# Kernel optimization log

Hardware: AMD Instinct MI355X
Metric: run time of the kernel (lower is better)

The kernel has to match this reference:

```python
import jax, jax.numpy as jnp
import numpy as np

N, C, H, W = 128, 1024, 16, 16
D_IN, L, D_OUT, NQ = 2048, 512, 1024, 16


def setup_inputs() -> dict:
    key = jax.random.key(0)
    k1, k2, k3, k4, k5 = jax.random.split(key, 5)
    return {
        "cat_tensor": jax.random.normal(k1, (N, C, H, W), dtype=jnp.float32),
        "context": jax.random.normal(k2, (N, D_IN, L), dtype=jnp.float32),
        "query": jax.random.normal(k3, (1, NQ, D_IN), dtype=jnp.float32),
        "W_in": jax.random.normal(k4, (D_IN, D_IN), dtype=jnp.float32) * (1.0 / np.sqrt(D_IN)),
        "W_out": jax.random.normal(k5, (D_OUT, 2 * D_IN), dtype=jnp.float32) * (1.0 / np.sqrt(2 * D_IN)),
    }


def reference(cat_tensor, context, query, W_in, W_out):
    n, c, h, w = cat_tensor.shape
    # AttnBlock: context comes in as [N, D_in, L] -> transpose to [N, L, D_in]
    ctx = jnp.swapaxes(context, 1, 2)  # [N, L, D]
    # learned query broadcast over batch, then 'general' projection (Linear, no bias)
    q = jnp.einsum('nqd,ed->nqe', jnp.broadcast_to(query, (n,) + query.shape[1:]), W_in)  # [N, Q, D]
    scores = jnp.einsum('nqd,nld->nql', q, ctx)            # [N, Q, L]
    weights = jax.nn.softmax(scores, axis=-1)              # [N, Q, L]
    mix = jnp.einsum('nql,nld->nqd', weights, ctx)         # [N, Q, D]
    combined = jnp.concatenate([mix, q], axis=-1)          # [N, Q, 2D]
    out = jnp.tanh(jnp.einsum('nqe,oe->nqo', combined, W_out))  # [N, Q, D_out]
    # reshape queries to a small spatial map: [N, D_out, Hq, Hq]
    hq = int(np.sqrt(out.shape[1]))
    amap = jnp.swapaxes(out, 1, 2).reshape(n, out.shape[2], hq, hq)
    # F.interpolate(..., (H, W)) default mode='nearest': idx = floor(i * in / out)
    ih = (jnp.arange(h) * hq) // h
    iw = (jnp.arange(w) * hq) // w
    amap = amap[:, :, ih, :][:, :, :, iw]                  # [N, D_out, H, W]
    return jnp.concatenate([cat_tensor, amap], axis=1)     # [N, C + D_out, H, W]
```

## Files before the change

### kernel.cpp

```cpp
#include <hip/hip_runtime.h>
#include <hip/hip_bf16.h>

#define NB   128
#define CIN  1024
#define HW   256
#define DIN  2048
#define LL   512
#define DOUT 1024
#define NQ   16

#define SC   8

typedef __attribute__((ext_vector_type(8))) short bf16x8;
typedef __attribute__((ext_vector_type(4))) float f32x4;

__global__ __launch_bounds__(256) void k_q(const float* __restrict__ query,
                                           const float* __restrict__ Win,
                                           float* __restrict__ qT) {
  int e    = blockIdx.x * 4 + (threadIdx.x >> 6);
  int lane = threadIdx.x & 63;
  const float* wr = Win + (size_t)e * DIN;
  float acc[16];
  #pragma unroll
  for (int qi = 0; qi < 16; ++qi) acc[qi] = 0.f;
  #pragma unroll 2
  for (int d = lane; d < DIN; d += 64) {
    float w = wr[d];
    #pragma unroll
    for (int qi = 0; qi < 16; ++qi) acc[qi] += w * query[qi * DIN + d];
  }
  #pragma unroll
  for (int qi = 0; qi < 16; ++qi) {
    float a = acc[qi];
    #pragma unroll
    for (int m = 32; m; m >>= 1) a += __shfl_xor(a, m);
    if (lane == 0) qT[e * 16 + qi] = a;
  }
}

__global__ __launch_bounds__(256) void k_qfill(const float* __restrict__ qT,
                                               __hip_bfloat16* __restrict__ comb) {
  int idx = blockIdx.x * 256 + threadIdx.x;
  int m = idx >> 8, e0 = (idx & 255) * 8;
  int qi = m & 15;
  union { bf16x8 v; __hip_bfloat16 h[8]; } u;
  #pragma unroll
  for (int j = 0; j < 8; ++j) u.h[j] = __float2bfloat16(qT[(e0 + j) * 16 + qi]);
  *(bf16x8*)&comb[(size_t)m * (2 * DIN) + DIN + e0] = u.v;
}

__global__ __launch_bounds__(256) void k_wcast(const float* __restrict__ W,
                                               __hip_bfloat16* __restrict__ Wb) {
  int idx = blockIdx.x * 256 + threadIdx.x;
  const float4* W4 = (const float4*)W;
  float4 a = W4[idx * 2], b = W4[idx * 2 + 1];
  union { bf16x8 v; __hip_bfloat16 h[8]; } u;
  u.h[0] = __float2bfloat16(a.x); u.h[1] = __float2bfloat16(a.y);
  u.h[2] = __float2bfloat16(a.z); u.h[3] = __float2bfloat16(a.w);
  u.h[4] = __float2bfloat16(b.x); u.h[5] = __float2bfloat16(b.y);
  u.h[6] = __float2bfloat16(b.z); u.h[7] = __float2bfloat16(b.w);
  *(bf16x8*)&Wb[(size_t)idx * 8] = u.v;
}

__global__ __launch_bounds__(256) void k_scores(const float* __restrict__ ctx,
                                                const float* __restrict__ qT,
                                                float* __restrict__ part) {
  int n = blockIdx.x, c = blockIdx.y, t = threadIdx.x;
  const int DS = DIN / SC;
  const float* cn  = ctx + (size_t)n * DIN * LL + (size_t)c * DS * LL;
  const float* qTc = qT + (size_t)c * DS * 16;
  float2 acc[16];
  #pragma unroll
  for (int qi = 0; qi < 16; ++qi) acc[qi] = make_float2(0.f, 0.f);
  #pragma unroll 4
  for (int d = 0; d < DS; ++d) {
    float2 v = *(const float2*)&cn[(size_t)d * LL + 2 * t];
    const float* qr = qTc + d * 16;
    #pragma unroll
    for (int qi = 0; qi < 16; ++qi) {
      acc[qi].x += qr[qi] * v.x;
      acc[qi].y += qr[qi] * v.y;
    }
  }
  float* po = part + (size_t)(c * NB + n) * 16 * LL;
  #pragma unroll
  for (int qi = 0; qi < 16; ++qi)
    *(float2*)&po[qi * LL + 2 * t] = acc[qi];
}

__global__ __launch_bounds__(256) void k_softmax(const float* __restrict__ part,
                                                 float* __restrict__ wT) {
  int b = blockIdx.x, n = b >> 4, qi = b & 15, t = threadIdx.x;
  __shared__ float red[256];
  float sc0 = 0.f, sc1 = 0.f;
  #pragma unroll
  for (int c = 0; c < SC; ++c) {
    const float* p = part + ((size_t)(c * NB + n) * 16 + qi) * LL;
    sc0 += p[t];
    sc1 += p[t + 256];
  }
  red[t] = fmaxf(sc0, sc1);
  __syncthreads();
  for (int s = 128; s; s >>= 1) { if (t < s) red[t] = fmaxf(red[t], red[t + s]); __syncthreads(); }
  float M = red[0];
  __syncthreads();
  float e0 = expf(sc0 - M), e1 = expf(sc1 - M);
  red[t] = e0 + e1;
  __syncthreads();
  for (int s = 128; s; s >>= 1) { if (t < s) red[t] += red[t + s]; __syncthreads(); }
  float inv = 1.0f / red[0];
  wT[((size_t)n * LL + t) * 16 + qi]       = e0 * inv;
  wT[((size_t)n * LL + t + 256) * 16 + qi] = e1 * inv;
}

__global__ __launch_bounds__(256) void k_mix(const float* __restrict__ ctx,
                                             const float* __restrict__ wT,
                                             __hip_bfloat16* __restrict__ comb) {
  int dt = blockIdx.x, n = blockIdx.y, t = threadIdx.x;
  int dbase = dt * 256;
  __shared__ float tile[256 * 33];
  const float* cn = ctx + (size_t)n * DIN * LL;
  const float* wn = wT + (size_t)n * LL * 16;
  const float* src0 = cn + (size_t)dbase * LL;
  float acc[16];
  #pragma unroll
  for (int qi = 0; qi < 16; ++qi) acc[qi] = 0.f;

  int lq = (t & 7) * 4;
  int row0 = t >> 3;

  float4 g[8];
  #pragma unroll
  for (int p = 0; p < 8; ++p)
    g[p] = *(const float4*)&src0[(size_t)(row0 + p * 32) * LL + lq];

  for (int ch = 0; ch < 16; ++ch) {
    __syncthreads();
    #pragma unroll
    for (int p = 0; p < 8; ++p) {
      int row = row0 + p * 32;
      float* dst = &tile[row * 33 + lq];
      dst[0] = g[p].x; dst[1] = g[p].y; dst[2] = g[p].z; dst[3] = g[p].w;
    }
    __syncthreads();
    if (ch < 15) {
      int l0n = (ch + 1) * 32;
      #pragma unroll
      for (int p = 0; p < 8; ++p)
        g[p] = *(const float4*)&src0[(size_t)(row0 + p * 32) * LL + l0n + lq];
    }
    int l0 = ch * 32;
    for (int l = 0; l < 32; ++l) {
      float v = tile[t * 33 + l];
      const float* wr = wn + (size_t)(l0 + l) * 16;
      #pragma unroll
      for (int qi = 0; qi < 16; ++qi) acc[qi] += wr[qi] * v;
    }
  }
  #pragma unroll
  for (int qi = 0; qi < 16; ++qi)
    comb[(size_t)(n * 16 + qi) * (2 * DIN) + dbase + t] = __float2bfloat16(acc[qi]);
}

__global__ __launch_bounds__(256) void k_gemm(const __hip_bfloat16* __restrict__ A,
                                              const __hip_bfloat16* __restrict__ B,
                                              float* __restrict__ out) {
  __shared__ short la[64 * 40];
  __shared__ short lb[64 * 40];
  int t = threadIdx.x, lane = t & 63, wid = t >> 6;
  int m0 = blockIdx.y * 64, o0 = blockIdx.x * 64;
  int wy = wid >> 1, wx = wid & 1;
  f32x4 acc[2][2] = {};
  int srow = t >> 2, sq = (t & 3) * 8;
  const short* As = (const short*)A;
  const short* Bs = (const short*)B;

  float4 ga = *(const float4*)&As[(size_t)(m0 + srow) * (2 * DIN) + sq];
  float4 gb = *(const float4*)&Bs[(size_t)(o0 + srow) * (2 * DIN) + sq];

  for (int kc = 0; kc < 2 * DIN; kc += 32) {
    __syncthreads();
    *(float4*)&la[srow * 40 + sq] = ga;
    *(float4*)&lb[srow * 40 + sq] = gb;
    __syncthreads();
    if (kc + 32 < 2 * DIN) {
      ga = *(const float4*)&As[(size_t)(m0 + srow) * (2 * DIN) + kc + 32 + sq];
      gb = *(const float4*)&Bs[(size_t)(o0 + srow) * (2 * DIN) + kc + 32 + sq];
    }
    int fr = lane & 15, fq = (lane >> 4) * 8;
    bf16x8 a0 = *(const bf16x8*)&la[(wy * 32 + fr) * 40 + fq];
    bf16x8 a1 = *(const bf16x8*)&la[(wy * 32 + 16 + fr) * 40 + fq];
    bf16x8 b0 = *(const bf16x8*)&lb[(wx * 32 + fr) * 40 + fq];
    bf16x8 b1 = *(const bf16x8*)&lb[(wx * 32 + 16 + fr) * 40 + fq];
    acc[0][0] = __builtin_amdgcn_mfma_f32_16x16x32_bf16(a0, b0, acc[0][0], 0, 0, 0);
    acc[0][1] = __builtin_amdgcn_mfma_f32_16x16x32_bf16(a0, b1, acc[0][1], 0, 0, 0);
    acc[1][0] = __builtin_amdgcn_mfma_f32_16x16x32_bf16(a1, b0, acc[1][0], 0, 0, 0);
    acc[1][1] = __builtin_amdgcn_mfma_f32_16x16x32_bf16(a1, b1, acc[1][1], 0, 0, 0);
  }

  int col = lane & 15, rbase = (lane >> 4) * 4;
  #pragma unroll
  for (int si = 0; si < 2; ++si)
    #pragma unroll
    for (int sj = 0; sj < 2; ++sj)
      #pragma unroll
      for (int r = 0; r < 4; ++r) {
        int m = m0 + wy * 32 + si * 16 + rbase + r;
        int o = o0 + wx * 32 + sj * 16 + col;
        float v = tanhf(acc[si][sj][r]);
        int n = m >> 4, qi = m & 15;
        float* op = out + (size_t)(n * 2048 + CIN + o) * HW
                        + ((qi >> 2) * 4) * 16 + (qi & 3) * 4;
        float4 vv = make_float4(v, v, v, v);
        *(float4*)&op[0]  = vv;
        *(float4*)&op[16] = vv;
        *(float4*)&op[32] = vv;
        *(float4*)&op[48] = vv;
      }
}

__global__ __launch_bounds__(256) void k_copy(const float* __restrict__ cat,
                                              float* __restrict__ out) {
  size_t idx = (size_t)blockIdx.x * 256 + threadIdx.x;
  int n = (int)(idx >> 16);
  int rem = (int)(idx & 65535);
  const float4* c4 = (const float4*)cat;
  float4* o4 = (float4*)out;
  o4[(size_t)n * 131072 + rem] = c4[idx];
}

extern "C" void kernel_launch(void* const* d_in, const int* in_sizes, int n_in,
                              void* d_out, int out_size, void* d_ws, size_t ws_size,
                              hipStream_t stream) {
  const float* cat   = (const float*)d_in[0];
  const float* ctx   = (const float*)d_in[1];
  const float* query = (const float*)d_in[2];
  const float* W_in  = (const float*)d_in[3];
  const float* W_out = (const float*)d_in[4];
  float* out = (float*)d_out;

  float* qT   = (float*)d_ws;
  float* wT   = qT + 32768;
  float* part = wT + 1048576;
  __hip_bfloat16* Wb   = (__hip_bfloat16*)(part + 8388608);
  __hip_bfloat16* comb = Wb + 4194304;

  k_q      <<<512, 256, 0, stream>>>(query, W_in, qT);
  k_wcast  <<<2048, 256, 0, stream>>>(W_out, Wb);
  k_qfill  <<<2048, 256, 0, stream>>>(qT, comb);
  k_scores <<<dim3(128, SC), 256, 0, stream>>>(ctx, qT, part);
  k_softmax<<<2048, 256, 0, stream>>>(part, wT);
  k_mix    <<<dim3(8, 128), 256, 0, stream>>>(ctx, wT, comb);
  k_gemm   <<<dim3(16, 32), 256, 0, stream>>>(comb, Wb, out);
  k_copy   <<<32768, 256, 0, stream>>>(cat, out);
}
```

Before: 1.093 ms.

## Precompute batch-invariant query half of output GEMM as bias; chunk attention by batch

```diff
diff --git a/kernel.cpp b/kernel.cpp
--- a/kernel.cpp
+++ b/kernel.cpp
@@ -9,7 +9,8 @@
 #define DOUT 1024
 #define NQ   16
 
-#define SC   8
+#define SC   16
+#define NQTR 32
 
 typedef __attribute__((ext_vector_type(8))) short bf16x8;
 typedef __attribute__((ext_vector_type(4))) float f32x4;
@@ -38,41 +39,53 @@
   }
 }
 
-__global__ __launch_bounds__(256) void k_qfill(const float* __restrict__ qT,
-                                               __hip_bfloat16* __restrict__ comb) {
-  int idx = blockIdx.x * 256 + threadIdx.x;
-  int m = idx >> 8, e0 = (idx & 255) * 8;
-  int qi = m & 15;
-  union { bf16x8 v; __hip_bfloat16 h[8]; } u;
-  #pragma unroll
-  for (int j = 0; j < 8; ++j) u.h[j] = __float2bfloat16(qT[(e0 + j) * 16 + qi]);
-  *(bf16x8*)&comb[(size_t)m * (2 * DIN) + DIN + e0] = u.v;
+__global__ __launch_bounds__(256) void k_bias(const float* __restrict__ qT,
+                                              const float* __restrict__ W,
+                                              float* __restrict__ bias) {
+  int o    = blockIdx.x * 4 + (threadIdx.x >> 6);
+  int lane = threadIdx.x & 63;
+  const float* wr = W + (size_t)o * (2 * DIN) + DIN;
+  float acc[16];
+  #pragma unroll
+  for (int qi = 0; qi < 16; ++qi) acc[qi] = 0.f;
+  for (int e = lane; e < DIN; e += 64) {
+    float w = wr[e];
+    #pragma unroll
+    for (int qi = 0; qi < 16; ++qi) acc[qi] += w * qT[e * 16 + qi];
+  }
+  #pragma unroll
+  for (int qi = 0; qi < 16; ++qi) {
+    float a = acc[qi];
+    #pragma unroll
+    for (int m = 32; m; m >>= 1) a += __shfl_xor(a, m);
+    if (lane == 0) bias[o * 16 + qi] = a;
+  }
 }
 
 __global__ __launch_bounds__(256) void k_wcast(const float* __restrict__ W,
                                                __hip_bfloat16* __restrict__ Wb) {
   int idx = blockIdx.x * 256 + threadIdx.x;
-  const float4* W4 = (const float4*)W;
-  float4 a = W4[idx * 2], b = W4[idx * 2 + 1];
+  int o = idx >> 8, e0 = (idx & 255) * 8;
+  const float* src = W + (size_t)o * (2 * DIN) + e0;
   union { bf16x8 v; __hip_bfloat16 h[8]; } u;
-  u.h[0] = __float2bfloat16(a.x); u.h[1] = __float2bfloat16(a.y);
-  u.h[2] = __float2bfloat16(a.z); u.h[3] = __float2bfloat16(a.w);
-  u.h[4] = __float2bfloat16(b.x); u.h[5] = __float2bfloat16(b.y);
-  u.h[6] = __float2bfloat16(b.z); u.h[7] = __float2bfloat16(b.w);
-  *(bf16x8*)&Wb[(size_t)idx * 8] = u.v;
+  #pragma unroll
+  for (int j = 0; j < 8; ++j) u.h[j] = __float2bfloat16(src[j]);
+  *(bf16x8*)&Wb[(size_t)o * DIN + e0] = u.v;
 }
 
 __global__ __launch_bounds__(256) void k_scores(const float* __restrict__ ctx,
                                                 const float* __restrict__ qT,
-                                                float* __restrict__ part) {
-  int n = blockIdx.x, c = blockIdx.y, t = threadIdx.x;
+                                                float* __restrict__ part,
+                                                int nbase) {
+  int bn = blockIdx.x, c = blockIdx.y, t = threadIdx.x;
+  int n = nbase + bn;
   const int DS = DIN / SC;
   const float* cn  = ctx + (size_t)n * DIN * LL + (size_t)c * DS * LL;
   const float* qTc = qT + (size_t)c * DS * 16;
   float2 acc[16];
   #pragma unroll
   for (int qi = 0; qi < 16; ++qi) acc[qi] = make_float2(0.f, 0.f);
-  #pragma unroll 4
+  #pragma unroll 8
   for (int d = 0; d < DS; ++d) {
     float2 v = *(const float2*)&cn[(size_t)d * LL + 2 * t];
     const float* qr = qTc + d * 16;
@@ -82,20 +95,22 @@
       acc[qi].y += qr[qi] * v.y;
     }
   }
-  float* po = part + (size_t)(c * NB + n) * 16 * LL;
+  float* po = part + (size_t)(c * NQTR + bn) * 16 * LL;
   #pragma unroll
   for (int qi = 0; qi < 16; ++qi)
     *(float2*)&po[qi * LL + 2 * t] = acc[qi];
 }
 
 __global__ __launch_bounds__(256) void k_softmax(const float* __restrict__ part,
-                                                 float* __restrict__ wT) {
-  int b = blockIdx.x, n = b >> 4, qi = b & 15, t = threadIdx.x;
+                                                 float* __restrict__ wT,
+                                                 int nbase) {
+  int b = blockIdx.x, bn = b >> 4, qi = b & 15, t = threadIdx.x;
+  int n = nbase + bn;
   __shared__ float red[256];
   float sc0 = 0.f, sc1 = 0.f;
   #pragma unroll
   for (int c = 0; c < SC; ++c) {
-    const float* p = part + ((size_t)(c * NB + n) * 16 + qi) * LL;
+    const float* p = part + ((size_t)(c * NQTR + bn) * 16 + qi) * LL;
     sc0 += p[t];
     sc1 += p[t + 256];
   }
@@ -115,8 +130,9 @@
 
 __global__ __launch_bounds__(256) void k_mix(const float* __restrict__ ctx,
                                              const float* __restrict__ wT,
-                                             __hip_bfloat16* __restrict__ comb) {
-  int dt = blockIdx.x, n = blockIdx.y, t = threadIdx.x;
+                                             __hip_bfloat16* __restrict__ comb,
+                                             int nbase) {
+  int dt = blockIdx.x, n = nbase + blockIdx.y, t = threadIdx.x;
   int dbase = dt * 256;
   __shared__ float tile[256 * 33];
   const float* cn = ctx + (size_t)n * DIN * LL;
@@ -159,43 +175,53 @@
   }
   #pragma unroll
   for (int qi = 0; qi < 16; ++qi)
-    comb[(size_t)(n * 16 + qi) * (2 * DIN) + dbase + t] = __float2bfloat16(acc[qi]);
+    comb[(size_t)(n * 16 + qi) * DIN + dbase + t] = __float2bfloat16(acc[qi]);
 }
 
 __global__ __launch_bounds__(256) void k_gemm(const __hip_bfloat16* __restrict__ A,
                                               const __hip_bfloat16* __restrict__ B,
+                                              const float* __restrict__ bias,
                                               float* __restrict__ out) {
-  __shared__ short la[64 * 40];
-  __shared__ short lb[64 * 40];
+  __shared__ short la[64 * 72];
+  __shared__ short lb[64 * 72];
   int t = threadIdx.x, lane = t & 63, wid = t >> 6;
   int m0 = blockIdx.y * 64, o0 = blockIdx.x * 64;
   int wy = wid >> 1, wx = wid & 1;
   f32x4 acc[2][2] = {};
-  int srow = t >> 2, sq = (t & 3) * 8;
+  int srow = t >> 2, sq = (t & 3) * 16;
   const short* As = (const short*)A;
   const short* Bs = (const short*)B;
 
-  float4 ga = *(const float4*)&As[(size_t)(m0 + srow) * (2 * DIN) + sq];
-  float4 gb = *(const float4*)&Bs[(size_t)(o0 + srow) * (2 * DIN) + sq];
-
-  for (int kc = 0; kc < 2 * DIN; kc += 32) {
-    __syncthreads();
-    *(float4*)&la[srow * 40 + sq] = ga;
-    *(float4*)&lb[srow * 40 + sq] = gb;
-    __syncthreads();
-    if (kc + 32 < 2 * DIN) {
-      ga = *(const float4*)&As[(size_t)(m0 + srow) * (2 * DIN) + kc + 32 + sq];
-      gb = *(const float4*)&Bs[(size_t)(o0 + srow) * (2 * DIN) + kc + 32 + sq];
+  float4 ga0 = *(const float4*)&As[(size_t)(m0 + srow) * DIN + sq];
+  float4 ga1 = *(const float4*)&As[(size_t)(m0 + srow) * DIN + sq + 8];
+  float4 gb0 = *(const float4*)&Bs[(size_t)(o0 + srow) * DIN + sq];
+  float4 gb1 = *(const float4*)&Bs[(size_t)(o0 + srow) * DIN + sq + 8];
+
+  for (int kc = 0; kc < DIN; kc += 64) {
+    __syncthreads();
+    *(float4*)&la[srow * 72 + sq]     = ga0;
+    *(float4*)&la[srow * 72 + sq + 8] = ga1;
+    *(float4*)&lb[srow * 72 + sq]     = gb0;
+    *(float4*)&lb[srow * 72 + sq + 8] = gb1;
+    __syncthreads();
+    if (kc + 64 < DIN) {
+      ga0 = *(const float4*)&As[(size_t)(m0 + srow) * DIN + kc + 64 + sq];
+      ga1 = *(const float4*)&As[(size_t)(m0 + srow) * DIN + kc + 64 + sq + 8];
+      gb0 = *(const float4*)&Bs[(size_t)(o0 + srow) * DIN + kc + 64 + sq];
+      gb1 = *(const float4*)&Bs[(size_t)(o0 + srow) * DIN + kc + 64 + sq + 8];
     }
     int fr = lane & 15, fq = (lane >> 4) * 8;
-    bf16x8 a0 = *(const bf16x8*)&la[(wy * 32 + fr) * 40 + fq];
-    bf16x8 a1 = *(const bf16x8*)&la[(wy * 32 + 16 + fr) * 40 + fq];
-    bf16x8 b0 = *(const bf16x8*)&lb[(wx * 32 + fr) * 40 + fq];
-    bf16x8 b1 = *(const bf16x8*)&lb[(wx * 32 + 16 + fr) * 40 + fq];
-    acc[0][0] = __builtin_amdgcn_mfma_f32_16x16x32_bf16(a0, b0, acc[0][0], 0, 0, 0);
-    acc[0][1] = __builtin_amdgcn_mfma_f32_16x16x32_bf16(a0, b1, acc[0][1], 0, 0, 0);
-    acc[1][0] = __builtin_amdgcn_mfma_f32_16x16x32_bf16(a1, b0, acc[1][0], 0, 0, 0);
-    acc[1][1] = __builtin_amdgcn_mfma_f32_16x16x32_bf16(a1, b1, acc[1][1], 0, 0, 0);
+    #pragma unroll
+    for (int kk = 0; kk < 64; kk += 32) {
+      bf16x8 a0 = *(const bf16x8*)&la[(wy * 32 + fr) * 72 + kk + fq];
+      bf16x8 a1 = *(const bf16x8*)&la[(wy * 32 + 16 + fr) * 72 + kk + fq];
+      bf16x8 b0 = *(const bf16x8*)&lb[(wx * 32 + fr) * 72 + kk + fq];
+      bf16x8 b1 = *(const bf16x8*)&lb[(wx * 32 + 16 + fr) * 72 + kk + fq];
+      acc[0][0] = __builtin_amdgcn_mfma_f32_16x16x32_bf16(a0, b0, acc[0][0], 0, 0, 0);
+      acc[0][1] = __builtin_amdgcn_mfma_f32_16x16x32_bf16(a0, b1, acc[0][1], 0, 0, 0);
+      acc[1][0] = __builtin_amdgcn_mfma_f32_16x16x32_bf16(a1, b0, acc[1][0], 0, 0, 0);
+      acc[1][1] = __builtin_amdgcn_mfma_f32_16x16x32_bf16(a1, b1, acc[1][1], 0, 0, 0);
+    }
   }
 
   int col = lane & 15, rbase = (lane >> 4) * 4;
@@ -207,8 +233,8 @@
       for (int r = 0; r < 4; ++r) {
         int m = m0 + wy * 32 + si * 16 + rbase + r;
         int o = o0 + wx * 32 + sj * 16 + col;
-        float v = tanhf(acc[si][sj][r]);
         int n = m >> 4, qi = m & 15;
+        float v = tanhf(acc[si][sj][r] + bias[o * 16 + qi]);
         float* op = out + (size_t)(n * 2048 + CIN + o) * HW
                         + ((qi >> 2) * 4) * 16 + (qi & 3) * 4;
         float4 vv = make_float4(v, v, v, v);
@@ -242,15 +268,21 @@
   float* qT   = (float*)d_ws;
   float* wT   = qT + 32768;
   float* part = wT + 1048576;
-  __hip_bfloat16* Wb   = (__hip_bfloat16*)(part + 8388608);
-  __hip_bfloat16* comb = Wb + 4194304;
-
-  k_q      <<<512, 256, 0, stream>>>(query, W_in, qT);
-  k_wcast  <<<2048, 256, 0, stream>>>(W_out, Wb);
-  k_qfill  <<<2048, 256, 0, stream>>>(qT, comb);
-  k_scores <<<dim3(128, SC), 256, 0, stream>>>(ctx, qT, part);
-  k_softmax<<<2048, 256, 0, stream>>>(part, wT);
-  k_mix    <<<dim3(8, 128), 256, 0, stream>>>(ctx, wT, comb);
-  k_gemm   <<<dim3(16, 32), 256, 0, stream>>>(comb, Wb, out);
-  k_copy   <<<32768, 256, 0, stream>>>(cat, out);
-}
+  float* bias = part + 4194304;
+  __hip_bfloat16* Wb   = (__hip_bfloat16*)(bias + 16384);
+  __hip_bfloat16* comb = Wb + 2097152;
+
+  k_copy  <<<32768, 256, 0, stream>>>(cat, out);
+  k_q     <<<512, 256, 0, stream>>>(query, W_in, qT);
+  k_wcast <<<1024, 256, 0, stream>>>(W_out, Wb);
+  k_bias  <<<256, 256, 0, stream>>>(qT, W_out, bias);
+
+  for (int q = 0; q < 4; ++q) {
+    int nbase = q * NQTR;
+    k_scores <<<dim3(NQTR, SC), 256, 0, stream>>>(ctx, qT, part, nbase);
+    k_softmax<<<NQTR * 16, 256, 0, stream>>>(part, wT, nbase);
+    k_mix    <<<dim3(8, NQTR), 256, 0, stream>>>(ctx, wT, comb, nbase);
+  }
+
+  k_gemm <<<dim3(16, 32), 256, 0, stream>>>(comb, Wb, bias, out);
+}
```

Measured after the change: 1.273 ms. +16.4%, slower.
